# Kernel tuning notes

Hardware: AMD Instinct MI355X
Metric: run time of the kernel (lower is better)

The kernel has to match this reference:

```python
import jax, jax.numpy as jnp
import numpy as np

K_SIM_SCHEDULE = [4, 8, 16]
K_CON_SCHEDULE = [2, 4, 8]
NEG = 1000000000.0


def _dual_adjacency(h, k_sim, k_con):
    """Binary causal dual adjacency (similar / dissimilar), no gradient."""
    B, T, D = h.shape
    h = jax.lax.stop_gradient(h)
    xn = h / jnp.maximum(jnp.linalg.norm(h, axis=-1, keepdims=True), 1e-12)
    sim = jnp.einsum('btd,bsd->bts', xn, xn)                 # (B,T,T)
    past = jnp.tril(jnp.ones((T, T), h.dtype), -1)           # strictly-past mask
    sim = sim * past - NEG * (1.0 - past)
    eff_sim = min(k_sim, T - 1)
    eff_con = min(k_con, max(0, T - 1 - eff_sim))
    bI = jnp.arange(B)[:, None, None]
    tI = jnp.arange(T)[None, :, None]
    A_sim = jnp.zeros((B, T, T), h.dtype)
    if eff_sim > 0:
        _, top_idx = jax.lax.top_k(sim, eff_sim)             # (B,T,k)
        A_sim = A_sim.at[bI, tI, top_idx].set(1.0) * past
    A_con = jnp.zeros((B, T, T), h.dtype)
    if eff_con > 0:
        sim_con = jnp.where(A_sim > 0, NEG, sim)
        _, bot_idx = jax.lax.top_k(-sim_con, eff_con)        # smallest eff_con
        A_con = A_con.at[bI, tI, bot_idx].set(1.0) * past * (1.0 - A_sim)
    return A_sim, A_con


def _aggregate(h, A):
    # unweighted mean over selected neighbors; empty rows -> zeros
    deg = jnp.sum(A, axis=-1, keepdims=True)
    return jnp.einsum('bts,bsd->btd', A, h) / jnp.maximum(deg, 1.0)


def setup_inputs() -> dict:
    key = jax.random.key(0)
    ks = jax.random.split(key, 2)
    B, T, D, R = 4, 2048, 512, 3
    x = jax.random.normal(ks[0], (B, T, D), dtype=jnp.float32)
    gain = jnp.ones((R, D), dtype=jnp.float32)
    bias = jnp.zeros((R, D), dtype=jnp.float32)
    log_mix = jnp.zeros((R,), dtype=jnp.float32)
    log_alpha = jnp.zeros((R,), dtype=jnp.float32)
    log_momentum = jnp.asarray(1.0, dtype=jnp.float32)
    log_scale = jnp.asarray(0.0, dtype=jnp.float32)
    return {"x": x, "gain": gain, "bias": bias, "log_mix": log_mix,
            "log_alpha": log_alpha, "log_momentum": log_momentum,
            "log_scale": log_scale}


def reference(x, gain, bias, log_mix, log_alpha, log_momentum, log_scale):
    momentum = jax.nn.sigmoid(log_momentum)
    scale = jax.nn.softplus(log_scale) + 0.01
    h = x
    for r in range(len(K_SIM_SCHEDULE)):
        mix = jax.nn.sigmoid(log_mix[r])
        alpha = jax.nn.sigmoid(log_alpha[r])
        A_sim, A_con = _dual_adjacency(h, K_SIM_SCHEDULE[r], K_CON_SCHEDULE[r])
        msg_pos = _aggregate(h, A_sim)
        msg_neg = _aggregate(h, A_con)
        ctx = alpha * msg_pos + (1.0 - alpha) * msg_neg
        blended = mix * h + (1.0 - mix) * ctx
        h_new = jax.nn.gelu(blended * gain[r] + bias[r], approximate=False)
        h = momentum * h + (1.0 - momentum) * h_new
    return (h - x) * scale
```

## Files before the change

kernel.cpp:

```cpp
#include <hip/hip_runtime.h>
#include <hip/hip_bf16.h>
#include <cstdint>
#include <cstddef>

#define BB 4
#define TT 2048
#define DD 512
#define NEG_INF (-3.402823466e+38f)
#define POS_INF (3.402823466e+38f)

typedef __attribute__((ext_vector_type(8))) short bf16x8;
typedef __attribute__((ext_vector_type(8))) unsigned short ushort8;
typedef __attribute__((ext_vector_type(4))) float f32x4;

__device__ __forceinline__ float sigmoidf_(float x){ return 1.0f/(1.0f+expf(-x)); }

__device__ __forceinline__ unsigned short f2bf(float x){
  __hip_bfloat16 b = __float2bfloat16(x);
  return *reinterpret_cast<unsigned short*>(&b);
}

__device__ __forceinline__ unsigned int fwd_map(float f){
  unsigned int b = __float_as_uint(f);
  return b ^ ((b & 0x80000000u) ? 0xFFFFFFFFu : 0x80000000u);
}
__device__ __forceinline__ float inv_map(unsigned int u){
  unsigned int b = (u & 0x80000000u) ? (u ^ 0x80000000u) : ~u;
  return __uint_as_float(b);
}

__global__ __launch_bounds__(64) void k_normsplit(const float* __restrict__ h, float* __restrict__ rnorm,
                                                  unsigned short* __restrict__ Xh, unsigned short* __restrict__ Xl){
  int row = blockIdx.x;
  const float* hr = h + (size_t)row*DD;
  int lane = threadIdx.x;
  float4 v0 = *(const float4*)&hr[lane*4];
  float4 v1 = *(const float4*)&hr[lane*4 + 256];
  float ss = v0.x*v0.x+v0.y*v0.y+v0.z*v0.z+v0.w*v0.w
           + v1.x*v1.x+v1.y*v1.y+v1.z*v1.z+v1.w*v1.w;
  #pragma unroll
  for (int off=32; off; off>>=1) ss += __shfl_xor(ss, off);
  float rn = 1.0f / fmaxf(sqrtf(ss), 1e-12f);
  if (lane==0) rnorm[row] = rn;

  float xs[8] = {v0.x,v0.y,v0.z,v0.w,v1.x,v1.y,v1.z,v1.w};
  unsigned short hb[8], lb[8];
  #pragma unroll
  for (int q=0;q<8;q++){
    float xn = xs[q]*rn;
    unsigned short hh = f2bf(xn);
    __hip_bfloat16 bh = *reinterpret_cast<__hip_bfloat16*>(&hh);
    float rem = xn - __bfloat162float(bh);
    hb[q] = hh; lb[q] = f2bf(rem);
  }
  ushort4 h0 = {hb[0],hb[1],hb[2],hb[3]}, h1 = {hb[4],hb[5],hb[6],hb[7]};
  ushort4 l0 = {lb[0],lb[1],lb[2],lb[3]}, l1 = {lb[4],lb[5],lb[6],lb[7]};
  *(ushort4*)&Xh[(size_t)row*DD + lane*4]       = h0;
  *(ushort4*)&Xh[(size_t)row*DD + lane*4 + 256] = h1;
  *(ushort4*)&Xl[(size_t)row*DD + lane*4]       = l0;
  *(ushort4*)&Xl[(size_t)row*DD + lane*4 + 256] = l1;
}

__global__ __launch_bounds__(256) void k_sim(const unsigned short* __restrict__ Xh,
                                             const unsigned short* __restrict__ Xl,
                                             float* __restrict__ sim, int b0){
  int p = blockIdx.x;
  int jt = (int)((sqrtf(8.0f*(float)p + 1.0f) - 1.0f)*0.5f);
  while ((jt+1)*(jt+2)/2 <= p) jt++;
  while (jt*(jt+1)/2 > p) jt--;
  int is = p - jt*(jt+1)/2;

  int bl = blockIdx.y;
  size_t xoff = (size_t)(b0 + bl)*TT*DD;
  const unsigned short* XhB = Xh + xoff;
  const unsigned short* XlB = Xl + xoff;
  float* simb = sim + (size_t)bl*TT*TT;
  int t0 = jt*128, s0 = is*128;

  __shared__ __align__(16) short As[128*32];
  __shared__ __align__(16) short Bs[128*32];

  int tid = threadIdx.x, wave = tid>>6, lane = tid&63;
  int wr = wave>>1, wc = wave&1;

  int srow = tid>>2;
  int sc8  = (tid&3)*8;

  f32x4 acc[4][4];
  #pragma unroll
  for (int m=0;m<4;m++)
    #pragma unroll
    for (int n=0;n<4;n++) acc[m][n] = (f32x4){0.f,0.f,0.f,0.f};

  ushort8 ra0, ra1, rb0, rb1;
  auto gload = [&](int s){
    int pass = s>>4; int kcol = (s&15)*32;
    const unsigned short* sA = (pass<2) ? XhB : XlB;
    const unsigned short* sB = (pass!=1) ? XhB : XlB;
    ra0 = *(const ushort8*)&sA[(size_t)(t0+srow)*DD + kcol + sc8];
    ra1 = *(const ushort8*)&sA[(size_t)(t0+srow+64)*DD + kcol + sc8];
    rb0 = *(const ushort8*)&sB[(size_t)(s0+srow)*DD + kcol + sc8];
    rb1 = *(const ushort8*)&sB[(size_t)(s0+srow+64)*DD + kcol + sc8];
  };

  gload(0);
  for (int s=0; s<48; ++s){
    __syncthreads();
    *(ushort8*)&As[srow*32 + sc8]      = ra0;
    *(ushort8*)&As[(srow+64)*32 + sc8] = ra1;
    *(ushort8*)&Bs[srow*32 + sc8]      = rb0;
    *(ushort8*)&Bs[(srow+64)*32 + sc8] = rb1;
    __syncthreads();
    if (s < 47) gload(s+1);

    int arow = wr*64 + (lane&15);
    int brow = wc*64 + (lane&15);
    int kb = (lane>>4)*8;
    bf16x8 af[4], bf[4];
    #pragma unroll
    for (int m=0;m<4;m++) af[m] = *(const bf16x8*)&As[(arow + m*16)*32 + kb];
    #pragma unroll
    for (int n=0;n<4;n++) bf[n] = *(const bf16x8*)&Bs[(brow + n*16)*32 + kb];
    #pragma unroll
    for (int m=0;m<4;m++)
      #pragma unroll
      for (int n=0;n<4;n++)
        acc[m][n] = __builtin_amdgcn_mfma_f32_16x16x32_bf16(af[m], bf[n], acc[m][n], 0, 0, 0);
  }

  #pragma unroll
  for (int m=0;m<4;m++){
    int t = t0 + wr*64 + m*16 + (lane>>4)*4;
    #pragma unroll
    for (int n=0;n<4;n++){
      int sc = s0 + wc*64 + n*16 + (lane&15);
      float* dst = simb + (size_t)t*TT + sc;
      #pragma unroll
      for (int j=0;j<4;j++) dst[(size_t)j*TT] = acc[m][n][j];
    }
  }
}

template<int ESIM, int ECON>
__global__ __launch_bounds__(256) void k_topk(const float* __restrict__ sim, int b0,
                                              const float* __restrict__ h, const float* __restrict__ rnorm,
                                              int* __restrict__ topidx, int* __restrict__ botidx,
                                              int* __restrict__ bcnt){
  constexpr int K1 = ESIM + 8;
  constexpr float TAU = 5e-5f;
  __shared__ unsigned int s_u[TT];
  __shared__ int s_hist[256];
  __shared__ int s_cand[K1];
  __shared__ int s_eq[44];
  __shared__ int s_sel[ESIM];
  __shared__ int s_bot[ECON + 8];
  __shared__ unsigned int s_pfx;
  __shared__ int s_kp, s_ngt, s_neq;

  int tid = threadIdx.x, lane = tid & 63, wid = tid >> 6;
  int lrow = blockIdx.x;
  int bl = lrow >> 11, t = lrow & (TT-1);
  int gb = b0 + bl;
  int grow = (gb << 11) | t;

  if (t <= ESIM){
    if (tid < t) topidx[(size_t)grow*16 + tid] = tid;
    if (tid == 0) bcnt[grow] = 0;
    return;
  }
  const float* srow = sim + (size_t)lrow*TT;
  const float* hb  = h + (size_t)gb*TT*DD;
  const float* rnb = rnorm + (size_t)gb*TT;

  for (int s = tid; s < t; s += 256) s_u[s] = fwd_map(srow[s]);
  int k1 = min(t, K1);
  if (tid == 0){ s_pfx = 0u; s_kp = k1; s_ngt = 0; s_neq = 0; }
  __syncthreads();

  for (int pass = 0; pass < 4; ++pass){
    int shift = 24 - 8*pass;
    unsigned int keep = (pass == 0) ? 0u : (0xFFFFFFFFu << (shift + 8));
    unsigned int pfx = s_pfx; int kp = s_kp;
    s_hist[tid] = 0;
    __syncthreads();
    for (int s = tid; s < t; s += 256){
      unsigned int u = s_u[s];
      if (((u ^ pfx) & keep) == 0)
        atomicAdd(&s_hist[(u >> shift) & 255], 1);
    }
    __syncthreads();
    if (wid == 0){
      int m4 = s_hist[4*lane] + s_hist[4*lane+1] + s_hist[4*lane+2] + s_hist[4*lane+3];
      int x = __shfl(m4, 63 - lane);
      #pragma unroll
      for (int off = 1; off < 64; off <<= 1){
        int v = __shfl_up(x, off);
        if (lane >= off) x += v;
      }
      int T = __shfl(x, 63 - lane);
      int G = T - m4;
      bool hit = (G < kp) && (kp <= T);
      if (hit){
        int c = G; int D = 4*lane;
        #pragma unroll
        for (int i = 3; i >= 0; --i){
          int hc = s_hist[4*lane + i];
          if (kp <= c + hc){ D = 4*lane + i; break; }
          c += hc;
        }
        s_pfx = pfx | ((unsigned int)D << shift);
        s_kp = kp - c;
      }
    }
    __syncthreads();
  }
  unsigned int uthr = s_pfx;

  for (int s = tid; s < t; s += 256){
    unsigned int u = s_u[s];
    if (u > uthr){
      int p = atomicAdd(&s_ngt, 1);
      s_cand[p] = s;
    } else if (u == uthr){
      int p = atomicAdd(&s_neq, 1);
      if (p < 44) s_eq[p] = s;
    }
  }
  __syncthreads();
  if (wid != 0) return;

  int c_gt = s_ngt;
  int c_eq = min(s_neq, 44);
  int ncand = min(c_gt + c_eq, 64);

  unsigned int myu = 0u; int myi = 0x7fffffff;
  if (lane < ncand){
    myi = (lane < c_gt) ? s_cand[lane] : s_eq[lane - c_gt];
    myu = s_u[myi];
  }

  float vA = 0.f, vB = 0.f;
  {
    unsigned int cu = myu; int ci = myi;
    #pragma unroll
    for (int k = 0; k <= ESIM; ++k){
      unsigned int bu = cu; int bi = ci;
      #pragma unroll
      for (int off=32; off; off>>=1){
        unsigned int ou = __shfl_xor(bu, off); int oi = __shfl_xor(bi, off);
        if (ou > bu || (ou == bu && oi < bi)){ bu = ou; bi = oi; }
      }
      if (k < ESIM && lane == 0) s_sel[k] = bi;
      if (k == ESIM-1) vA = inv_map(bu);
      if (k == ESIM)   vB = inv_map(bu);
      if (ci == bi){ cu = 0u; ci = 0x7fffffff; }
    }
  }

  bool resc = (vA - vB < TAU);
  if (resc){
    const float* hq = hb + (size_t)t*DD;
    float rt = rnb[t];
    float4 q0 = *(const float4*)&hq[lane*4];
    float4 q1 = *(const float4*)&hq[lane*4 + 256];
    float ev = NEG_INF;
    for (int j = 0; j < ncand; ++j){
      int idx = (j < c_gt) ? s_cand[j] : s_eq[j - c_gt];
      const float* hc = hb + (size_t)idx*DD;
      float4 c0 = *(const float4*)&hc[lane*4];
      float4 c1 = *(const float4*)&hc[lane*4 + 256];
      float pp = q0.x*c0.x+q0.y*c0.y+q0.z*c0.z+q0.w*c0.w
               + q1.x*c1.x+q1.y*c1.y+q1.z*c1.z+q1.w*c1.w;
      #pragma unroll
      for (int off=32; off; off>>=1) pp += __shfl_xor(pp, off);
      float ex = pp * rt * rnb[idx];
      if (lane == j) ev = ex;
    }
    float rv = (lane < ncand) ? ev : NEG_INF;
    int   ri = myi;
    #pragma unroll
    for (int k = 0; k < ESIM; ++k){
      float bv = rv; int bi = ri;
      #pragma unroll
      for (int off=32; off; off>>=1){
        float ov = __shfl_xor(bv, off); int oi = __shfl_xor(bi, off);
        if (ov > bv || (ov == bv && oi < bi)){ bv = ov; bi = oi; }
      }
      if (lane == 0) s_sel[k] = bi;
      if (ri == bi) rv = NEG_INF;
    }
  }
  if (lane < ESIM) topidx[(size_t)grow*16 + lane] = s_sel[lane];

  int need = ECON - (TT - t);
  int cnt = 0;
  if (need > 0){
    if (lane < ESIM) s_u[s_sel[lane]] = 0xFFFFFFFFu;
    int nb_ext = min(need + 8, t - ESIM);
    float wA = 0.f, wB = 0.f;
    for (int k = 0; k < nb_ext; ++k){
      unsigned int mu = 0xFFFFFFFFu; int mi = 0x7fffffff;
      for (int s = lane; s < t; s += 64){
        unsigned int u = s_u[s];
        if (u < mu || (u == mu && s < mi)){ mu = u; mi = s; }
      }
      #pragma unroll
      for (int off=32; off; off>>=1){
        unsigned int ou = __shfl_xor(mu, off); int oi = __shfl_xor(mi, off);
        if (ou < mu || (ou == mu && oi < mi)){ mu = ou; mi = oi; }
      }
      if (lane == 0){ s_bot[k] = mi; s_u[mi] = 0xFFFFFFFFu; }
      if (k == need-1) wA = inv_map(mu);
      if (k == need)   wB = inv_map(mu);
    }
    cnt = need;
    bool rb = (nb_ext > need) && (wB - wA < TAU);
    if (!rb){
      if (lane < need) botidx[(size_t)grow*8 + lane] = s_bot[lane];
    } else {
      const float* hq = hb + (size_t)t*DD;
      float rt = rnb[t];
      float4 q0 = *(const float4*)&hq[lane*4];
      float4 q1 = *(const float4*)&hq[lane*4 + 256];
      float ev = POS_INF; int ei = 0x7fffffff;
      for (int j = 0; j < nb_ext; ++j){
        int idx = s_bot[j];
        const float* hc = hb + (size_t)idx*DD;
        float4 c0 = *(const float4*)&hc[lane*4];
        float4 c1 = *(const float4*)&hc[lane*4 + 256];
        float pp = q0.x*c0.x+q0.y*c0.y+q0.z*c0.z+q0.w*c0.w
                 + q1.x*c1.x+q1.y*c1.y+q1.z*c1.z+q1.w*c1.w;
        #pragma unroll
        for (int off=32; off; off>>=1) pp += __shfl_xor(pp, off);
        float ex = pp * rt * rnb[idx];
        if (lane == j){ ev = ex; ei = idx; }
      }
      #pragma unroll
      for (int k = 0; k < ECON; ++k){
        if (k < need){
          float bv = ev; int bi = ei;
          #pragma unroll
          for (int off=32; off; off>>=1){
            float ov = __shfl_xor(bv, off); int oi = __shfl_xor(bi, off);
            if (ov < bv || (ov == bv && oi < bi)){ bv = ov; bi = oi; }
          }
          if (lane == 0) botidx[(size_t)grow*8 + k] = bi;
          if (ei == bi) ev = POS_INF;
        }
      }
    }
  }
  if (lane == 0) bcnt[grow] = cnt;
}

__global__ __launch_bounds__(256) void k_agg(const float* __restrict__ hsrc, float* __restrict__ hdst,
                                             const int* __restrict__ topidx, const int* __restrict__ botidx,
                                             const int* __restrict__ bcnt,
                                             const float* __restrict__ gain, const float* __restrict__ bias,
                                             const float* __restrict__ log_mix, const float* __restrict__ log_alpha,
                                             const float* __restrict__ log_momentum, int r, int eff_sim){
  int row = blockIdx.x;
  int b = row >> 11; int t = row & (TT-1);
  int n_sim = min(eff_sim, t);
  int n_con = bcnt[row];
  float mix      = sigmoidf_(log_mix[r]);
  float alpha    = sigmoidf_(log_alpha[r]);
  float momentum = sigmoidf_(log_momentum[0]);
  const float* hb = hsrc + (size_t)b*TT*DD;

  __shared__ int sidx[16];
  __shared__ int scidx[8];
  if (threadIdx.x < 16) sidx[threadIdx.x]  = (threadIdx.x < n_sim) ? topidx[(size_t)row*16 + threadIdx.x] : 0;
  if (threadIdx.x < 8)  scidx[threadIdx.x] = (threadIdx.x < n_con) ? botidx[(size_t)row*8  + threadIdx.x] : 0;
  __syncthreads();

  #pragma unroll
  for (int e = threadIdx.x; e < DD; e += 256){
    float sp = 0.f;
    for (int j=0;j<n_sim;j++) sp += hb[(size_t)sidx[j]*DD + e];
    float sn = 0.f;
    for (int j=0;j<n_con;j++) sn += hb[(size_t)scidx[j]*DD + e];
    float mp = sp / (float)max(n_sim, 1);
    float mn = sn / (float)max(n_con, 1);
    float ctx = alpha*mp + (1.f-alpha)*mn;
    float hv = hsrc[(size_t)row*DD + e];
    float blended = mix*hv + (1.f-mix)*ctx;
    float u = blended*gain[e] + bias[e];
    float g = 0.5f*u*(1.0f + erff(u*0.7071067811865475f));
    hdst[(size_t)row*DD + e] = momentum*hv + (1.f-momentum)*g;
  }
}

__global__ __launch_bounds__(256) void k_final(const float* __restrict__ hfin, const float* __restrict__ x,
                                               const float* __restrict__ log_scale, float* __restrict__ out, int n){
  float scale = log1pf(expf(log_scale[0])) + 0.01f;
  int i = blockIdx.x*256 + threadIdx.x;
  if (i < n) out[i] = (hfin[i] - x[i]) * scale;
}

extern "C" void kernel_launch(void* const* d_in, const int* in_sizes, int n_in,
                              void* d_out, int out_size, void* d_ws, size_t ws_size,
                              hipStream_t stream) {
  const float* x         = (const float*)d_in[0];
  const float* gain      = (const float*)d_in[1];
  const float* bias      = (const float*)d_in[2];
  const float* log_mix   = (const float*)d_in[3];
  const float* log_alpha = (const float*)d_in[4];
  const float* log_mom   = (const float*)d_in[5];
  const float* log_scale = (const float*)d_in[6];

  float* hA = (float*)d_out;
  char* ws = (char*)d_ws;
  size_t off = 0;
  auto alloc = [&](size_t bytes){ void* p = ws + off; off += (bytes + 255) & ~(size_t)255; return p; };

  float*          hB     = (float*)alloc((size_t)BB*TT*DD*4);
  float*          rnorm  = (float*)alloc((size_t)BB*TT*4);
  int*            topidx = (int*)  alloc((size_t)BB*TT*16*4);
  int*            botidx = (int*)  alloc((size_t)BB*TT*8*4);
  int*            bcnt   = (int*)  alloc((size_t)BB*TT*4);
  unsigned short* Xh     = (unsigned short*)alloc((size_t)BB*TT*DD*2);
  unsigned short* Xl     = (unsigned short*)alloc((size_t)BB*TT*DD*2);

  size_t rem = (ws_size > off) ? (ws_size - off) : 0;
  int cb = (int)(rem / ((size_t)TT*TT*4));
  if (cb < 1) cb = 1;
  if (cb > BB) cb = BB;
  float* sim = (float*)alloc((size_t)cb*TT*TT*4);

  const float* hsrc = x;
  float* hdst = hB;
  const int ks[3] = {4, 8, 16};

  for (int r = 0; r < 3; ++r){
    k_normsplit<<<BB*TT, 64, 0, stream>>>(hsrc, rnorm, Xh, Xl);
    for (int b0 = 0; b0 < BB; b0 += cb){
      int nb = (BB - b0 < cb) ? (BB - b0) : cb;
      dim3 g(136, nb);
      k_sim<<<g, 256, 0, stream>>>(Xh, Xl, sim, b0);
      if (r == 0)      k_topk<4,2><<<nb*TT, 256, 0, stream>>>(sim, b0, hsrc, rnorm, topidx, botidx, bcnt);
      else if (r == 1) k_topk<8,4><<<nb*TT, 256, 0, stream>>>(sim, b0, hsrc, rnorm, topidx, botidx, bcnt);
      else             k_topk<16,8><<<nb*TT, 256, 0, stream>>>(sim, b0, hsrc, rnorm, topidx, botidx, bcnt);
    }
    k_agg<<<BB*TT, 256, 0, stream>>>(hsrc, hdst, topidx, botidx, bcnt,
                                     gain + (size_t)r*DD, bias + (size_t)r*DD,
                                     log_mix, log_alpha, log_mom, r, ks[r]);
    if (r == 0){ hsrc = hB; hdst = hA; }
    else if (r == 1){ hsrc = hA; hdst = hB; }
  }
  k_final<<<(BB*TT*DD)/256, 256, 0, stream>>>(hB, x, log_scale, (float*)d_out, BB*TT*DD);
}
```

Before: 550.0 us.

## Process one top-k row per wavefront instead of per workgroup

The top-k selection kernel now assigns each of the four wavefronts in a 256-thread block its own row, with per-wave shared-memory slices. Block-wide __syncthreads are replaced by wave-level shuffles and ballots for the radix-select passes. The first histogram is fused into the float4-vectorized load, and candidate compaction uses ballot/popcount instead of shared atomics. This targets barrier overhead and the three idle waves of the old design, at the cost of 4x shared memory per block, which may limit occupancy.

```diff
diff --git a/kernel.cpp b/kernel.cpp
--- a/kernel.cpp
+++ b/kernel.cpp
@@ -147,96 +147,128 @@
                                               int* __restrict__ topidx, int* __restrict__ botidx,
                                               int* __restrict__ bcnt){
   constexpr int K1 = ESIM + 8;
+  constexpr int EQCAP = 44;
   constexpr float TAU = 5e-5f;
-  __shared__ unsigned int s_u[TT];
-  __shared__ int s_hist[256];
-  __shared__ int s_cand[K1];
-  __shared__ int s_eq[44];
-  __shared__ int s_sel[ESIM];
-  __shared__ int s_bot[ECON + 8];
-  __shared__ unsigned int s_pfx;
-  __shared__ int s_kp, s_ngt, s_neq;
+  __shared__ unsigned int s_u[4][TT];
+  __shared__ int s_hist[4][256];
+  __shared__ int s_cand[4][K1];
+  __shared__ int s_eq[4][EQCAP];
+  __shared__ int s_sel[4][ESIM];
+  __shared__ int s_bot[4][ECON + 8];
 
   int tid = threadIdx.x, lane = tid & 63, wid = tid >> 6;
-  int lrow = blockIdx.x;
+  int lrow = blockIdx.x*4 + wid;
   int bl = lrow >> 11, t = lrow & (TT-1);
   int gb = b0 + bl;
   int grow = (gb << 11) | t;
 
   if (t <= ESIM){
-    if (tid < t) topidx[(size_t)grow*16 + tid] = tid;
-    if (tid == 0) bcnt[grow] = 0;
+    if (lane < t) topidx[(size_t)grow*16 + lane] = lane;
+    if (lane == 0) bcnt[grow] = 0;
     return;
   }
   const float* srow = sim + (size_t)lrow*TT;
   const float* hb  = h + (size_t)gb*TT*DD;
   const float* rnb = rnorm + (size_t)gb*TT;
 
-  for (int s = tid; s < t; s += 256) s_u[s] = fwd_map(srow[s]);
-  int k1 = min(t, K1);
-  if (tid == 0){ s_pfx = 0u; s_kp = k1; s_ngt = 0; s_neq = 0; }
-  __syncthreads();
-
+  unsigned int* su = s_u[wid];
+  int* sh = s_hist[wid];
+  int* scand = s_cand[wid];
+  int* seq   = s_eq[wid];
+  int* ssel  = s_sel[wid];
+  int* sbot  = s_bot[wid];
+
+  #pragma unroll
+  for (int i=0;i<4;i++) sh[lane + i*64] = 0;
+  int t4 = t & ~3;
+  for (int s4 = lane*4; s4 < t4; s4 += 256){
+    float4 f = *(const float4*)&srow[s4];
+    unsigned int u0=fwd_map(f.x), u1=fwd_map(f.y), u2=fwd_map(f.z), u3=fwd_map(f.w);
+    *(uint4*)&su[s4] = (uint4){u0,u1,u2,u3};
+    atomicAdd(&sh[u0>>24],1); atomicAdd(&sh[u1>>24],1);
+    atomicAdd(&sh[u2>>24],1); atomicAdd(&sh[u3>>24],1);
+  }
+  for (int s = t4 + lane; s < t; s += 64){
+    unsigned int u = fwd_map(srow[s]);
+    su[s] = u; atomicAdd(&sh[u>>24],1);
+  }
+
+  unsigned int pfx = 0u; int kp = min(t, K1);
+  #pragma unroll
   for (int pass = 0; pass < 4; ++pass){
     int shift = 24 - 8*pass;
-    unsigned int keep = (pass == 0) ? 0u : (0xFFFFFFFFu << (shift + 8));
-    unsigned int pfx = s_pfx; int kp = s_kp;
-    s_hist[tid] = 0;
-    __syncthreads();
-    for (int s = tid; s < t; s += 256){
-      unsigned int u = s_u[s];
-      if (((u ^ pfx) & keep) == 0)
-        atomicAdd(&s_hist[(u >> shift) & 255], 1);
-    }
-    __syncthreads();
-    if (wid == 0){
-      int m4 = s_hist[4*lane] + s_hist[4*lane+1] + s_hist[4*lane+2] + s_hist[4*lane+3];
-      int x = __shfl(m4, 63 - lane);
-      #pragma unroll
-      for (int off = 1; off < 64; off <<= 1){
-        int v = __shfl_up(x, off);
-        if (lane >= off) x += v;
-      }
-      int T = __shfl(x, 63 - lane);
-      int G = T - m4;
-      bool hit = (G < kp) && (kp <= T);
-      if (hit){
-        int c = G; int D = 4*lane;
-        #pragma unroll
-        for (int i = 3; i >= 0; --i){
-          int hc = s_hist[4*lane + i];
-          if (kp <= c + hc){ D = 4*lane + i; break; }
-          c += hc;
-        }
-        s_pfx = pfx | ((unsigned int)D << shift);
-        s_kp = kp - c;
-      }
-    }
-    __syncthreads();
-  }
-  unsigned int uthr = s_pfx;
-
-  for (int s = tid; s < t; s += 256){
-    unsigned int u = s_u[s];
-    if (u > uthr){
-      int p = atomicAdd(&s_ngt, 1);
-      s_cand[p] = s;
-    } else if (u == uthr){
-      int p = atomicAdd(&s_neq, 1);
-      if (p < 44) s_eq[p] = s;
-    }
-  }
-  __syncthreads();
-  if (wid != 0) return;
-
-  int c_gt = s_ngt;
-  int c_eq = min(s_neq, 44);
+    int m4 = sh[4*lane] + sh[4*lane+1] + sh[4*lane+2] + sh[4*lane+3];
+    int x = __shfl(m4, 63-lane);
+    #pragma unroll
+    for (int off = 1; off < 64; off <<= 1){
+      int v = __shfl_up(x, off);
+      if (lane >= off) x += v;
+    }
+    int T = __shfl(x, 63-lane);
+    int G = T - m4;
+    bool hit = (G < kp) && (kp <= T);
+    unsigned int npfx = 0u; int nkp = 0;
+    if (hit){
+      int c = G; int D = 4*lane;
+      #pragma unroll
+      for (int i = 3; i >= 0; --i){
+        int hc = sh[4*lane + i];
+        if (kp <= c + hc){ D = 4*lane + i; break; }
+        c += hc;
+      }
+      npfx = pfx | ((unsigned int)D << shift);
+      nkp = kp - c;
+    }
+    unsigned long long hm = __ballot(hit);
+    int src = __ffsll(hm) - 1;
+    pfx = __shfl(npfx, src);
+    kp  = __shfl(nkp, src);
+    if (pass == 3) break;
+
+    int nshift = shift - 8;
+    unsigned int keep = 0xFFFFFFFFu << shift;
+    #pragma unroll
+    for (int i=0;i<4;i++) sh[lane + i*64] = 0;
+    for (int s4 = lane*4; s4 < t4; s4 += 256){
+      uint4 u = *(const uint4*)&su[s4];
+      if (((u.x ^ pfx) & keep) == 0) atomicAdd(&sh[(u.x>>nshift)&255],1);
+      if (((u.y ^ pfx) & keep) == 0) atomicAdd(&sh[(u.y>>nshift)&255],1);
+      if (((u.z ^ pfx) & keep) == 0) atomicAdd(&sh[(u.z>>nshift)&255],1);
+      if (((u.w ^ pfx) & keep) == 0) atomicAdd(&sh[(u.w>>nshift)&255],1);
+    }
+    for (int s = t4 + lane; s < t; s += 64){
+      unsigned int u = su[s];
+      if (((u ^ pfx) & keep) == 0) atomicAdd(&sh[(u>>nshift)&255],1);
+    }
+  }
+  unsigned int uthr = pfx;
+
+  int ngt = 0, neq = 0;
+  {
+    unsigned long long below = (lane == 0) ? 0ull : ((~0ull) >> (64 - lane));
+    for (int sb = 0; sb < t; sb += 64){
+      int s = sb + lane;
+      bool in = (s < t);
+      unsigned int u = in ? su[s] : 0u;
+      bool g = in && (u > uthr), e = in && (u == uthr);
+      unsigned long long mg = __ballot(g), me = __ballot(e);
+      if (g) scand[ngt + __popcll(mg & below)] = s;
+      if (e){
+        int pos = neq + __popcll(me & below);
+        if (pos < EQCAP) seq[pos] = s;
+      }
+      ngt += __popcll(mg); neq += __popcll(me);
+    }
+  }
+
+  int c_gt = ngt;
+  int c_eq = min(neq, EQCAP);
   int ncand = min(c_gt + c_eq, 64);
 
   unsigned int myu = 0u; int myi = 0x7fffffff;
   if (lane < ncand){
-    myi = (lane < c_gt) ? s_cand[lane] : s_eq[lane - c_gt];
-    myu = s_u[myi];
+    myi = (lane < c_gt) ? scand[lane] : seq[lane - c_gt];
+    myu = su[myi];
   }
 
   float vA = 0.f, vB = 0.f;
@@ -250,7 +282,7 @@
         unsigned int ou = __shfl_xor(bu, off); int oi = __shfl_xor(bi, off);
         if (ou > bu || (ou == bu && oi < bi)){ bu = ou; bi = oi; }
       }
-      if (k < ESIM && lane == 0) s_sel[k] = bi;
+      if (k < ESIM && lane == 0) ssel[k] = bi;
       if (k == ESIM-1) vA = inv_map(bu);
       if (k == ESIM)   vB = inv_map(bu);
       if (ci == bi){ cu = 0u; ci = 0x7fffffff; }
@@ -265,7 +297,7 @@
     float4 q1 = *(const float4*)&hq[lane*4 + 256];
     float ev = NEG_INF;
     for (int j = 0; j < ncand; ++j){
-      int idx = (j < c_gt) ? s_cand[j] : s_eq[j - c_gt];
+      int idx = (j < c_gt) ? scand[j] : seq[j - c_gt];
       const float* hc = hb + (size_t)idx*DD;
       float4 c0 = *(const float4*)&hc[lane*4];
       float4 c1 = *(const float4*)&hc[lane*4 + 256];
@@ -286,22 +318,22 @@
         float ov = __shfl_xor(bv, off); int oi = __shfl_xor(bi, off);
         if (ov > bv || (ov == bv && oi < bi)){ bv = ov; bi = oi; }
       }
-      if (lane == 0) s_sel[k] = bi;
+      if (lane == 0) ssel[k] = bi;
       if (ri == bi) rv = NEG_INF;
     }
   }
-  if (lane < ESIM) topidx[(size_t)grow*16 + lane] = s_sel[lane];
+  if (lane < ESIM) topidx[(size_t)grow*16 + lane] = ssel[lane];
 
   int need = ECON - (TT - t);
   int cnt = 0;
   if (need > 0){
-    if (lane < ESIM) s_u[s_sel[lane]] = 0xFFFFFFFFu;
+    if (lane < ESIM) su[ssel[lane]] = 0xFFFFFFFFu;
     int nb_ext = min(need + 8, t - ESIM);
     float wA = 0.f, wB = 0.f;
     for (int k = 0; k < nb_ext; ++k){
       unsigned int mu = 0xFFFFFFFFu; int mi = 0x7fffffff;
       for (int s = lane; s < t; s += 64){
-        unsigned int u = s_u[s];
+        unsigned int u = su[s];
         if (u < mu || (u == mu && s < mi)){ mu = u; mi = s; }
       }
       #pragma unroll
@@ -309,14 +341,14 @@
         unsigned int ou = __shfl_xor(mu, off); int oi = __shfl_xor(mi, off);
         if (ou < mu || (ou == mu && oi < mi)){ mu = ou; mi = oi; }
       }
-      if (lane == 0){ s_bot[k] = mi; s_u[mi] = 0xFFFFFFFFu; }
+      if (lane == 0){ sbot[k] = mi; su[mi] = 0xFFFFFFFFu; }
       if (k == need-1) wA = inv_map(mu);
       if (k == need)   wB = inv_map(mu);
     }
     cnt = need;
     bool rb = (nb_ext > need) && (wB - wA < TAU);
     if (!rb){
-      if (lane < need) botidx[(size_t)grow*8 + lane] = s_bot[lane];
+      if (lane < need) botidx[(size_t)grow*8 + lane] = sbot[lane];
     } else {
       const float* hq = hb + (size_t)t*DD;
       float rt = rnb[t];
@@ -324,7 +356,7 @@
       float4 q1 = *(const float4*)&hq[lane*4 + 256];
       float ev = POS_INF; int ei = 0x7fffffff;
       for (int j = 0; j < nb_ext; ++j){
-        int idx = s_bot[j];
+        int idx = sbot[j];
         const float* hc = hb + (size_t)idx*DD;
         float4 c0 = *(const float4*)&hc[lane*4];
         float4 c1 = *(const float4*)&hc[lane*4 + 256];
@@ -438,9 +470,9 @@
       int nb = (BB - b0 < cb) ? (BB - b0) : cb;
       dim3 g(136, nb);
       k_sim<<<g, 256, 0, stream>>>(Xh, Xl, sim, b0);
-      if (r == 0)      k_topk<4,2><<<nb*TT, 256, 0, stream>>>(sim, b0, hsrc, rnorm, topidx, botidx, bcnt);
-      else if (r == 1) k_topk<8,4><<<nb*TT, 256, 0, stream>>>(sim, b0, hsrc, rnorm, topidx, botidx, bcnt);
-      else             k_topk<16,8><<<nb*TT, 256, 0, stream>>>(sim, b0, hsrc, rnorm, topidx, botidx, bcnt);
+      if (r == 0)      k_topk<4,2><<<nb*TT/4, 256, 0, stream>>>(sim, b0, hsrc, rnorm, topidx, botidx, bcnt);
+      else if (r == 1) k_topk<8,4><<<nb*TT/4, 256, 0, stream>>>(sim, b0, hsrc, rnorm, topidx, botidx, bcnt);
+      else             k_topk<16,8><<<nb*TT/4, 256, 0, stream>>>(sim, b0, hsrc, rnorm, topidx, botidx, bcnt);
     }
     k_agg<<<BB*TT, 256, 0, stream>>>(hsrc, hdst, topidx, botidx, bcnt,
                                      gain + (size_t)r*DD, bias + (size_t)r*DD,
```

After: 552.2 us. About the same (+0.4%).
